# Optimization experiments

Measured on AMD Instinct MI355X. Metric: run time of the kernel, lower is better.

The kernel has to match this reference:

```python
import jax, jax.numpy as jnp
import numpy as np

N, E, B, V, ED, M = 100000, 1600000, 100, 10000, 16, 64
EPS = 1e-5

def _seg_mean(x, ids, n):
    s = jax.ops.segment_sum(x, ids, num_segments=n)
    c = jax.ops.segment_sum(jnp.ones((x.shape[0], 1), x.dtype), ids, num_segments=n)
    return s / jnp.maximum(c, 1.0)

def _graph_conv(x, src, dst, ew, w_rel, b_rel, w_root):
    # PyG GraphConv: out = lin_rel(sum_j e_ji * x_j) + lin_root(x)
    msg = x[src] * ew[:, None]                       # [E, din] gather + weight
    agg = jax.ops.segment_sum(msg, dst, num_segments=x.shape[0])  # scatter-add
    return agg @ w_rel + b_rel + x @ w_root

def _graph_norm(x, batch, g, b, a):
    m = _seg_mean(x, batch, B)
    xc = x - a * m[batch]
    v = _seg_mean(xc * xc, batch, B)
    return g * xc / jnp.sqrt(v[batch] + EPS) + b

def _lrelu(x):
    return jnp.where(x > 0, x, 0.01 * x)

def _bn(x, g, b):
    m = x.mean(0)
    v = x.var(0)
    return g * (x - m) / jnp.sqrt(v + EPS) + b

def setup_inputs() -> dict:
    key = jax.random.key(0)
    ks = jax.random.split(key, 36)
    def lin(k, din, dout):
        return jax.random.normal(k, (din, dout), jnp.float32) / np.sqrt(din)
    d = {
        'x_idx': jax.random.randint(ks[0], (N,), 0, V),
        'edge_index': jax.random.randint(ks[1], (2, E), 0, N),
        'edge_attr': jax.random.uniform(ks[2], (E, 1), jnp.float32),
        'batch': jnp.sort(jax.random.randint(ks[3], (N,), 0, B)),
        'demographics': jax.random.normal(ks[4], (B, 4), jnp.float32),
        'emb': jax.random.normal(ks[5], (V, ED), jnp.float32),
        'w_rel1': lin(ks[6], ED, M),   'b_rel1': jnp.zeros((M,), jnp.float32),   'w_root1': lin(ks[7], ED, M),
        'w_rel2': lin(ks[8], M, 2*M),  'b_rel2': jnp.zeros((2*M,), jnp.float32), 'w_root2': lin(ks[9], M, 2*M),
        'w_rel3': lin(ks[10], 2*M, 4*M),'b_rel3': jnp.zeros((4*M,), jnp.float32),'w_root3': lin(ks[11], 2*M, 4*M),
        'gn1_g': jnp.ones((M,), jnp.float32),   'gn1_b': jnp.zeros((M,), jnp.float32),   'gn1_a': jnp.ones((M,), jnp.float32),
        'gn2_g': jnp.ones((2*M,), jnp.float32), 'gn2_b': jnp.zeros((2*M,), jnp.float32), 'gn2_a': jnp.ones((2*M,), jnp.float32),
        'demo_w': lin(ks[12], 4, 16), 'demo_b': jnp.zeros((16,), jnp.float32),
        'l1_w': lin(ks[13], 4*M + 16, 2*M), 'l1_b': jnp.zeros((2*M,), jnp.float32),
        'bn1_g': jnp.ones((2*M,), jnp.float32), 'bn1_b': jnp.zeros((2*M,), jnp.float32),
        'l2_w': lin(ks[14], 2*M, M), 'l2_b': jnp.zeros((M,), jnp.float32),
        'bn2_g': jnp.ones((M,), jnp.float32), 'bn2_b': jnp.zeros((M,), jnp.float32),
        'l3_w': lin(ks[15], M, 3), 'l3_b': jnp.zeros((3,), jnp.float32),
    }
    return d

def reference(x_idx, edge_index, edge_attr, batch, demographics, emb,
              w_rel1, b_rel1, w_root1, w_rel2, b_rel2, w_root2, w_rel3, b_rel3, w_root3,
              gn1_g, gn1_b, gn1_a, gn2_g, gn2_b, gn2_a,
              demo_w, demo_b, l1_w, l1_b, bn1_g, bn1_b, l2_w, l2_b, bn2_g, bn2_b, l3_w, l3_b):
    src, dst = edge_index[0], edge_index[1]
    ew = edge_attr[:, 0]                  # squeeze(-1)
    x = emb[x_idx]                        # [N, 16]
    x = _graph_conv(x, src, dst, ew, w_rel1, b_rel1, w_root1)
    x = _lrelu(_graph_norm(x, batch, gn1_g, gn1_b, gn1_a))
    x = _graph_conv(x, src, dst, ew, w_rel2, b_rel2, w_root2)
    x = _lrelu(_graph_norm(x, batch, gn2_g, gn2_b, gn2_a))
    x = _graph_conv(x, src, dst, ew, w_rel3, b_rel3, w_root3)   # [N, 256]
    gf = _seg_mean(x, batch, B)                                  # global_mean_pool [B, 256]
    demo = demographics @ demo_w + demo_b                        # [B, 16]
    h = jnp.concatenate([gf, demo], axis=1)                      # [B, 272]
    h = _lrelu(_bn(h @ l1_w + l1_b, bn1_g, bn1_b))               # dropout = identity (eval)
    h = _lrelu(_bn(h @ l2_w + l2_b, bn2_g, bn2_b))
    return h @ l3_w + l3_b                                       # [B, 3]
```

## Files before the change

### kernel.cpp

```cpp
#include <hip/hip_runtime.h>

#define NN 100000
#define NE 1600000
#define NBATCH 100
#define NBUCK 391
constexpr float EPS = 1e-5f;

typedef unsigned short ushort_t;
typedef unsigned int uint_t;

using short8 = __attribute__((ext_vector_type(8))) short;
using floatx4 = __attribute__((ext_vector_type(4))) float;

__device__ __forceinline__ float lrelu(float x) { return x > 0.f ? x : 0.01f * x; }

__device__ __forceinline__ float b2f(ushort_t u) {
    union { uint_t i; float f; } c; c.i = ((uint_t)u) << 16; return c.f;
}
__device__ __forceinline__ ushort_t f2b(float f) {
    union { float f; uint_t i; } c; c.f = f;
    uint_t u = c.i;
    return (ushort_t)((u + 0x7FFFu + ((u >> 16) & 1u)) >> 16);
}
__device__ __forceinline__ void unpack8(const uint4 u, float* f) {
    f[0] = b2f(u.x & 0xffff); f[1] = b2f(u.x >> 16);
    f[2] = b2f(u.y & 0xffff); f[3] = b2f(u.y >> 16);
    f[4] = b2f(u.z & 0xffff); f[5] = b2f(u.z >> 16);
    f[6] = b2f(u.w & 0xffff); f[7] = b2f(u.w >> 16);
}


__global__ __launch_bounds__(256) void k_bcount(const int* __restrict__ dst,
                                                int* __restrict__ bcnt) {
    __shared__ int h[NBUCK];
    for (int i = threadIdx.x; i < NBUCK; i += 256) h[i] = 0;
    __syncthreads();
    for (int e = blockIdx.x * 256 + threadIdx.x; e < NE; e += gridDim.x * 256)
        atomicAdd(&h[dst[e] >> 8], 1);
    __syncthreads();
    for (int i = threadIdx.x; i < NBUCK; i += 256)
        if (h[i]) atomicAdd(&bcnt[i], h[i]);
}

__global__ __launch_bounds__(512) void k_bscan(const int* __restrict__ bcnt,
                                               int* __restrict__ bbase,
                                               int* __restrict__ bcur,
                                               int* __restrict__ rowstart) {
    __shared__ int s[512];
    const int t = threadIdx.x;
    const int v = (t < NBUCK) ? bcnt[t] : 0;
    s[t] = v;
    __syncthreads();
    for (int off = 1; off < 512; off <<= 1) {
        int o = (t >= off) ? s[t - off] : 0;
        __syncthreads();
        s[t] += o;
        __syncthreads();
    }
    const int excl = s[t] - v;
    if (t < NBUCK) { bbase[t] = excl; bcur[t] = excl; }
    if (t == 0) { bbase[NBUCK] = NE; rowstart[NN] = NE; }
}

__global__ __launch_bounds__(256) void k_bscatter(const int* __restrict__ dst,
                                                  const int* __restrict__ srcv,
                                                  const float* __restrict__ ew,
                                                  int* __restrict__ bcur,
                                                  int2* __restrict__ ebuf) {
    __shared__ int h[NBUCK];
    __shared__ int lcur[NBUCK];
    const int chunk = (NE + gridDim.x - 1) / gridDim.x;
    const int beg = blockIdx.x * chunk;
    const int end = (beg + chunk < NE) ? beg + chunk : NE;
    for (int i = threadIdx.x; i < NBUCK; i += 256) h[i] = 0;
    __syncthreads();
    for (int e = beg + threadIdx.x; e < end; e += 256)
        atomicAdd(&h[dst[e] >> 8], 1);
    __syncthreads();
    for (int i = threadIdx.x; i < NBUCK; i += 256)
        lcur[i] = h[i] ? atomicAdd(&bcur[i], h[i]) : 0;
    __syncthreads();
    for (int e = beg + threadIdx.x; e < end; e += 256) {
        const int d = dst[e];
        const int pos = atomicAdd(&lcur[d >> 8], 1);
        ebuf[pos] = make_int2(srcv[e] | ((d & 255) << 20), __float_as_int(ew[e]));
    }
}

__global__ __launch_bounds__(256) void k_bfinal(const int2* __restrict__ ebuf,
                                                const int* __restrict__ bbase,
                                                int* __restrict__ rowstart,
                                                int2* __restrict__ csr_pair) {
    __shared__ int h[256];
    __shared__ int cur[256];
    const int b = blockIdx.x;
    const int t = threadIdx.x;
    const int base = bbase[b];
    const int cnt = bbase[b + 1] - base;
    h[t] = 0;
    __syncthreads();
    for (int i = t; i < cnt; i += 256)
        atomicAdd(&h[(ebuf[base + i].x >> 20) & 255], 1);
    __syncthreads();
    const int v = h[t];
    cur[t] = v;
    __syncthreads();
    for (int off = 1; off < 256; off <<= 1) {
        int o = (t >= off) ? cur[t - off] : 0;
        __syncthreads();
        cur[t] += o;
        __syncthreads();
    }
    const int excl = cur[t] - v;
    const int n = (b << 8) + t;
    if (n < NN) rowstart[n] = base + excl;
    __syncthreads();
    cur[t] = excl;
    __syncthreads();
    for (int i = t; i < cnt; i += 256) {
        const int2 p = ebuf[base + i];
        const int loc = (p.x >> 20) & 255;
        const int pos = base + atomicAdd(&cur[loc], 1);
        csr_pair[pos] = make_int2(p.x & 0xFFFFF, p.y);
    }
}

__global__ void k_bounds(const int* __restrict__ batch, int* __restrict__ bstart) {
    int b = blockIdx.x * blockDim.x + threadIdx.x;
    if (b > NBATCH) return;
    int lo = 0, hi = NN;
    while (lo < hi) {
        int mid = (lo + hi) >> 1;
        if (batch[mid] < b) lo = mid + 1; else hi = mid;
    }
    bstart[b] = lo;
}


__global__ void k_wpack(const float* __restrict__ wr1, const float* __restrict__ wo1,
                        const float* __restrict__ wr2, const float* __restrict__ wo2,
                        const float* __restrict__ wr3, const float* __restrict__ wo3,
                        ushort_t* __restrict__ w1T, ushort_t* __restrict__ w2T,
                        ushort_t* __restrict__ w3T) {
    int idx = blockIdx.x * blockDim.x + threadIdx.x;
    if (idx < 2048) {
        int n = idx >> 5, k = idx & 31;
        float v = (k < 16) ? wr1[k * 64 + n] : wo1[(k - 16) * 64 + n];
        w1T[idx] = f2b(v);
    } else if (idx < 2048 + 16384) {
        int l = idx - 2048; int n = l >> 7, k = l & 127;
        float v = (k < 64) ? wr2[k * 128 + n] : wo2[(k - 64) * 128 + n];
        w2T[l] = f2b(v);
    } else if (idx < 2048 + 16384 + 65536) {
        int l = idx - 18432; int n = l >> 8, k = l & 255;
        float v = (k < 128) ? wr3[k * 256 + n] : wo3[(k - 128) * 256 + n];
        w3T[l] = f2b(v);
    }
}


__global__ void k_gather_b(const int* __restrict__ xi, const float* __restrict__ emb,
                           ushort_t* __restrict__ xcat0) {
    int n = blockIdx.x * blockDim.x + threadIdx.x;
    if (n >= NN) return;
    const float* e = emb + ((size_t)xi[n] << 4);
    uint_t u[8];
#pragma unroll
    for (int j = 0; j < 8; ++j)
        u[j] = (uint_t)f2b(e[2 * j]) | ((uint_t)f2b(e[2 * j + 1]) << 16);
    uint4* o = (uint4*)(xcat0 + (size_t)n * 32 + 16);
    o[0] = {u[0], u[1], u[2], u[3]};
    o[1] = {u[4], u[5], u[6], u[7]};
}


template <int D>
__global__ void k_aggregate_b(ushort_t* __restrict__ xcat, const int2* __restrict__ csr_pair,
                              const int* __restrict__ rowstart) {
    constexpr int LPN = D / 8;
    constexpr int EP = 64 / LPN;
    const int n = blockIdx.x * 4 + (threadIdx.x >> 6);
    const int lane = threadIdx.x & 63;
    const int sl = lane % LPN;
    const int eg = lane / LPN;
    if (n >= NN) return;
    const int beg = rowstart[n], end = rowstart[n + 1];
    float a0[8] = {}, a1[8] = {};
    int i = beg + eg;
    for (; i + EP < end; i += 2 * EP) {
        const int2 p0 = csr_pair[i];
        const int2 p1 = csr_pair[i + EP];
        const float w0 = __int_as_float(p0.y);
        const float w1 = __int_as_float(p1.y);
        const uint4 u0 = *(const uint4*)(xcat + (size_t)p0.x * (2 * D) + D + sl * 8);
        const uint4 u1 = *(const uint4*)(xcat + (size_t)p1.x * (2 * D) + D + sl * 8);
        float f0[8], f1[8];
        unpack8(u0, f0); unpack8(u1, f1);
#pragma unroll
        for (int j = 0; j < 8; ++j) { a0[j] += f0[j] * w0; a1[j] += f1[j] * w1; }
    }
    if (i < end) {
        const int2 p0 = csr_pair[i];
        const float w0 = __int_as_float(p0.y);
        const uint4 u0 = *(const uint4*)(xcat + (size_t)p0.x * (2 * D) + D + sl * 8);
        float f0[8];
        unpack8(u0, f0);
#pragma unroll
        for (int j = 0; j < 8; ++j) a0[j] += f0[j] * w0;
    }
#pragma unroll
    for (int j = 0; j < 8; ++j) a0[j] += a1[j];
#pragma unroll
    for (int m = LPN; m < 64; m <<= 1)
#pragma unroll
        for (int j = 0; j < 8; ++j) a0[j] += __shfl_xor(a0[j], m);
    if (eg == 0) {
        uint_t u[4];
#pragma unroll
        for (int j = 0; j < 4; ++j)
            u[j] = (uint_t)f2b(a0[2 * j]) | ((uint_t)f2b(a0[2 * j + 1]) << 16);
        *(uint4*)(xcat + (size_t)n * (2 * D) + sl * 8) = {u[0], u[1], u[2], u[3]};
    }
}


template <int K2, int DOUT, bool BOUT>
__global__ __launch_bounds__(256) void k_conv_mfma(
        const ushort_t* __restrict__ xcat, const ushort_t* __restrict__ wcatT,
        const float* __restrict__ brel, void* __restrict__ outp) {
    constexpr int CW = DOUT / 64;
    const int lane = threadIdx.x & 63;
    const int wv = threadIdx.x >> 6;
    const int m = lane & 15;
    const int quad = lane >> 4;
    const int r0 = blockIdx.x * 64;

    floatx4 acc[4][CW] = {};

    const ushort_t* arow[4];
#pragma unroll
    for (int r = 0; r < 4; ++r) {
        int an = r0 + r * 16 + m; if (an >= NN) an = NN - 1;
        arow[r] = xcat + (size_t)an * K2 + quad * 8;
    }
    const ushort_t* brow[CW];
#pragma unroll
    for (int c = 0; c < CW; ++c)
        brow[c] = wcatT + (size_t)((wv * CW + c) * 16 + m) * K2 + quad * 8;

    for (int kk = 0; kk < K2; kk += 32) {
        short8 a[4], b[CW];
#pragma unroll
        for (int r = 0; r < 4; ++r) a[r] = *(const short8*)(arow[r] + kk);
#pragma unroll
        for (int c = 0; c < CW; ++c) b[c] = *(const short8*)(brow[c] + kk);
#pragma unroll
        for (int r = 0; r < 4; ++r)
#pragma unroll
            for (int c = 0; c < CW; ++c)
                acc[r][c] = __builtin_amdgcn_mfma_f32_16x16x32_bf16(a[r], b[c], acc[r][c], 0, 0, 0);
    }

#pragma unroll
    for (int c = 0; c < CW; ++c) {
        const int col = (wv * CW + c) * 16 + m;
        const float bias = brel[col];
#pragma unroll
        for (int r = 0; r < 4; ++r) {
#pragma unroll
            for (int rr = 0; rr < 4; ++rr) {
                const int row = r0 + r * 16 + quad * 4 + rr;
                if (row < NN) {
                    const float v = acc[r][c][rr] + bias;
                    if constexpr (BOUT) ((ushort_t*)outp)[(size_t)row * DOUT + col] = f2b(v);
                    else                ((float*)outp)[(size_t)row * DOUT + col] = v;
                }
            }
        }
    }
}


template <int D, int OST>
__global__ __launch_bounds__(256) void k_graphnorm(
        const float* __restrict__ xf, ushort_t* __restrict__ xout,
        const int* __restrict__ bstart, const float* __restrict__ a,
        const float* __restrict__ g, const float* __restrict__ bb) {
    __shared__ float4 reds[256];
    __shared__ float4 redq[256];
    __shared__ float smean[64];
    __shared__ float sinv[64];
    const int b = blockIdx.x;
    const int col0 = blockIdx.y * 64;
    const int c4 = (threadIdx.x & 15) * 4;
    const int rg = threadIdx.x >> 4;
    const int beg = bstart[b], end = bstart[b + 1];
    const float cntf = fmaxf((float)(end - beg), 1.f);

    float4 s = {0.f, 0.f, 0.f, 0.f}, q = {0.f, 0.f, 0.f, 0.f};
    for (int r = beg + rg; r < end; r += 16) {
        const float4 v = *(const float4*)&xf[(size_t)r * D + col0 + c4];
        s.x += v.x; s.y += v.y; s.z += v.z; s.w += v.w;
        q.x += v.x * v.x; q.y += v.y * v.y; q.z += v.z * v.z; q.w += v.w * v.w;
    }
    reds[threadIdx.x] = s;
    redq[threadIdx.x] = q;
    __syncthreads();
    if (rg == 0) {
        float4 S = reds[threadIdx.x], Q = redq[threadIdx.x];
        for (int k = 1; k < 16; ++k) {
            const float4 s2 = reds[threadIdx.x + 16 * k];
            const float4 q2 = redq[threadIdx.x + 16 * k];
            S.x += s2.x; S.y += s2.y; S.z += s2.z; S.w += s2.w;
            Q.x += q2.x; Q.y += q2.y; Q.z += q2.z; Q.w += q2.w;
        }
        const float4 al = *(const float4*)&a[col0 + c4];
        const float Sv[4] = {S.x, S.y, S.z, S.w};
        const float Qv[4] = {Q.x, Q.y, Q.z, Q.w};
        const float av[4] = {al.x, al.y, al.z, al.w};
#pragma unroll
        for (int c = 0; c < 4; ++c) {
            const float mm = Sv[c] / cntf;
            const float ex2 = Qv[c] / cntf;
            const float var = fmaxf(ex2 - mm * mm * (2.f * av[c] - av[c] * av[c]), 0.f);
            smean[c4 + c] = mm;
            sinv[c4 + c] = 1.f / sqrtf(var + EPS);
        }
    }
    __syncthreads();
    const float4 mean4 = *(const float4*)&smean[c4];
    const float4 inv4 = *(const float4*)&sinv[c4];
    const float4 al4 = *(const float4*)&a[col0 + c4];
    const float4 g4 = *(const float4*)&g[col0 + c4];
    const float4 bb4 = *(const float4*)&bb[col0 + c4];
    for (int r = beg + rg; r < end; r += 16) {
        const float4 v = *(const float4*)&xf[(size_t)r * D + col0 + c4];
        float y0 = lrelu(g4.x * (v.x - al4.x * mean4.x) * inv4.x + bb4.x);
        float y1 = lrelu(g4.y * (v.y - al4.y * mean4.y) * inv4.y + bb4.y);
        float y2 = lrelu(g4.z * (v.z - al4.z * mean4.z) * inv4.z + bb4.z);
        float y3 = lrelu(g4.w * (v.w - al4.w * mean4.w) * inv4.w + bb4.w);
        uint2 o;
        o.x = (uint_t)f2b(y0) | ((uint_t)f2b(y1) << 16);
        o.y = (uint_t)f2b(y2) | ((uint_t)f2b(y3) << 16);
        *(uint2*)&xout[(size_t)r * OST + col0 + c4] = o;
    }
}


__global__ __launch_bounds__(256) void k_gf2b(const ushort_t* __restrict__ x3b,
                                              const int* __restrict__ bstart,
                                              float* __restrict__ h0) {
    __shared__ float4 red[256];
    const int b = blockIdx.x;
    const int col0 = blockIdx.y * 64;
    const int c4 = (threadIdx.x & 15) * 4;
    const int rg = threadIdx.x >> 4;
    const int beg = bstart[b], end = bstart[b + 1];
    const float cntf = fmaxf((float)(end - beg), 1.f);
    float4 s = {0.f, 0.f, 0.f, 0.f};
    for (int r = beg + rg; r < end; r += 16) {
        const uint2 u = *(const uint2*)&x3b[(size_t)r * 256 + col0 + c4];
        s.x += b2f(u.x & 0xffff); s.y += b2f(u.x >> 16);
        s.z += b2f(u.y & 0xffff); s.w += b2f(u.y >> 16);
    }
    red[threadIdx.x] = s;
    __syncthreads();
    if (rg == 0) {
        float4 S = red[threadIdx.x];
        for (int k = 1; k < 16; ++k) {
            const float4 s2 = red[threadIdx.x + 16 * k];
            S.x += s2.x; S.y += s2.y; S.z += s2.z; S.w += s2.w;
        }
        S.x /= cntf; S.y /= cntf; S.z /= cntf; S.w /= cntf;
        *(float4*)&h0[b * 272 + col0 + c4] = S;
    }
}

__global__ void k_demo(const float* __restrict__ dg, const float* __restrict__ w,
                       const float* __restrict__ b, float* __restrict__ h0) {
    int idx = blockIdx.x * blockDim.x + threadIdx.x;
    if (idx < NBATCH * 16) {
        int i = idx >> 4, j = idx & 15;
        float acc = b[j];
        for (int k = 0; k < 4; ++k) acc += dg[i * 4 + k] * w[k * 16 + j];
        h0[i * 272 + 256 + j] = acc;
    }
}

__global__ __launch_bounds__(128) void k_lin_bn(const float* __restrict__ in,
                                                const float* __restrict__ w,
                                                const float* __restrict__ bias,
                                                const float* __restrict__ g,
                                                const float* __restrict__ bb,
                                                float* __restrict__ out,
                                                int rows, int K, int C) {
    __shared__ float s1[128], s2[128];
    const int j = blockIdx.x;
    const int t = threadIdx.x;
    float v = 0.f;
    if (t < rows) {
        v = bias[j];
        for (int k = 0; k < K; ++k) v += in[t * K + k] * w[k * C + j];
    }
    s1[t] = (t < rows) ? v : 0.f;
    s2[t] = (t < rows) ? v * v : 0.f;
    __syncthreads();
    for (int off = 64; off > 0; off >>= 1) {
        if (t < off) { s1[t] += s1[t + off]; s2[t] += s2[t + off]; }
        __syncthreads();
    }
    const float m = s1[0] / rows;
    const float var = fmaxf(s2[0] / rows - m * m, 0.f);
    const float inv = 1.f / sqrtf(var + EPS);
    if (t < rows) out[t * C + j] = lrelu(g[j] * (v - m) * inv + bb[j]);
}

__global__ void k_linear(const float* __restrict__ in, const float* __restrict__ w,
                         const float* __restrict__ b, float* __restrict__ out,
                         int rows, int K, int D) {
    int total = rows * D;
    for (int idx = blockIdx.x * blockDim.x + threadIdx.x; idx < total; idx += gridDim.x * blockDim.x) {
        int i = idx / D, j = idx - i * D;
        float acc = b[j];
        for (int k = 0; k < K; ++k) acc += in[i * K + k] * w[k * D + j];
        out[idx] = acc;
    }
}


extern "C" void kernel_launch(void* const* d_in, const int* in_sizes, int n_in,
                              void* d_out, int out_size, void* d_ws, size_t ws_size,
                              hipStream_t stream) {
    const int*   x_idx  = (const int*)d_in[0];
    const int*   ei     = (const int*)d_in[1];
    const float* eattr  = (const float*)d_in[2];
    const int*   batch  = (const int*)d_in[3];
    const float* demog  = (const float*)d_in[4];
    const float* emb    = (const float*)d_in[5];
    const float* wrel1  = (const float*)d_in[6];
    const float* brel1  = (const float*)d_in[7];
    const float* wroot1 = (const float*)d_in[8];
    const float* wrel2  = (const float*)d_in[9];
    const float* brel2  = (const float*)d_in[10];
    const float* wroot2 = (const float*)d_in[11];
    const float* wrel3  = (const float*)d_in[12];
    const float* brel3  = (const float*)d_in[13];
    const float* wroot3 = (const float*)d_in[14];
    const float* gn1g = (const float*)d_in[15];
    const float* gn1b = (const float*)d_in[16];
    const float* gn1a = (const float*)d_in[17];
    const float* gn2g = (const float*)d_in[18];
    const float* gn2b = (const float*)d_in[19];
    const float* gn2a = (const float*)d_in[20];
    const float* dw   = (const float*)d_in[21];
    const float* db   = (const float*)d_in[22];
    const float* l1w  = (const float*)d_in[23];
    const float* l1b  = (const float*)d_in[24];
    const float* bn1g = (const float*)d_in[25];
    const float* bn1b = (const float*)d_in[26];
    const float* l2w  = (const float*)d_in[27];
    const float* l2b  = (const float*)d_in[28];
    const float* bn2g = (const float*)d_in[29];
    const float* bn2b = (const float*)d_in[30];
    const float* l3w  = (const float*)d_in[31];
    const float* l3b  = (const float*)d_in[32];
    float* out = (float*)d_out;

    float*    W     = (float*)d_ws;
    float*    xf    = W;
    int2*     ebuf  = (int2*)W;
    ushort_t* x3b   = (ushort_t*)(W + 12800000);
    ushort_t* xcat0 = (ushort_t*)(W + 25600000);
    ushort_t* xcat1 = (ushort_t*)(W + 27200000);
    ushort_t* xcat2 = (ushort_t*)(W + 33600000);
    ushort_t* w1T   = (ushort_t*)(W + 46400000);
    ushort_t* w2T   = w1T + 2048;
    ushort_t* w3T   = w2T + 16384;
    int2*     csr_pair = (int2*)(W + 46450000);
    int*      rowstart = (int*)(W + 49650000);
    int*      bstart   = (int*)(W + 49760000);
    int*      bcnt     = (int*)(W + 49761000);
    int*      bbase    = (int*)(W + 49762000);
    int*      bcur     = (int*)(W + 49763000);
    float*    h0 = W + 49770000;
    float*    h1 = h0 + 27200;
    float*    h2 = h1 + 12800;

    const int* src = ei;
    const int* dst = ei + NE;

    auto gsz = [](long long t) {
        long long b = (t + 255) / 256;
        return (int)(b > 524288 ? 524288 : b);
    };
    const int mfma_blk = (NN + 63) / 64;
    const int nagg_blk = (NN + 3) / 4;

    hipMemsetAsync(bcnt, 0, NBUCK * sizeof(int), stream);
    k_bcount<<<256, 256, 0, stream>>>(dst, bcnt);
    k_bscan<<<1, 512, 0, stream>>>(bcnt, bbase, bcur, rowstart);
    k_bscatter<<<256, 256, 0, stream>>>(dst, src, eattr, bcur, ebuf);
    k_bfinal<<<NBUCK, 256, 0, stream>>>(ebuf, bbase, rowstart, csr_pair);

    k_bounds<<<1, 128, 0, stream>>>(batch, bstart);
    k_wpack<<<(83968 + 255) / 256, 256, 0, stream>>>(wrel1, wroot1, wrel2, wroot2, wrel3, wroot3,
                                                     w1T, w2T, w3T);

    k_gather_b<<<(NN + 255) / 256, 256, 0, stream>>>(x_idx, emb, xcat0);

    k_aggregate_b<16><<<nagg_blk, 256, 0, stream>>>(xcat0, csr_pair, rowstart);
    k_conv_mfma<32, 64, false><<<mfma_blk, 256, 0, stream>>>(xcat0, w1T, brel1, xf);
    k_graphnorm<64, 128><<<dim3(NBATCH, 1), 256, 0, stream>>>(xf, xcat1 + 64, bstart, gn1a, gn1g, gn1b);

    k_aggregate_b<64><<<nagg_blk, 256, 0, stream>>>(xcat1, csr_pair, rowstart);
    k_conv_mfma<128, 128, false><<<mfma_blk, 256, 0, stream>>>(xcat1, w2T, brel2, xf);
    k_graphnorm<128, 256><<<dim3(NBATCH, 2), 256, 0, stream>>>(xf, xcat2 + 128, bstart, gn2a, gn2g, gn2b);

    k_aggregate_b<128><<<nagg_blk, 256, 0, stream>>>(xcat2, csr_pair, rowstart);
    k_conv_mfma<256, 256, true><<<mfma_blk, 256, 0, stream>>>(xcat2, w3T, brel3, x3b);

    k_gf2b<<<dim3(NBATCH, 4), 256, 0, stream>>>(x3b, bstart, h0);
    k_demo<<<(NBATCH * 16 + 255) / 256, 256, 0, stream>>>(demog, dw, db, h0);
    k_lin_bn<<<128, 128, 0, stream>>>(h0, l1w, l1b, bn1g, bn1b, h1, NBATCH, 272, 128);
    k_lin_bn<<<64, 128, 0, stream>>>(h1, l2w, l2b, bn2g, bn2b, h2, NBATCH, 128, 64);
    k_linear<<<gsz(NBATCH * 3), 256, 0, stream>>>(h2, l3w, l3b, out, NBATCH, 64, 3);
}
```

Before: 714.3 us.

## Fuse global mean pool into final conv MFMA epilogue via atomics

```diff
diff --git a/kernel.cpp b/kernel.cpp
--- a/kernel.cpp
+++ b/kernel.cpp
@@ -224,10 +224,12 @@
 }
 
 
-template <int K2, int DOUT, bool BOUT>
+template <int K2, int DOUT, int MODE>
 __global__ __launch_bounds__(256) void k_conv_mfma(
         const ushort_t* __restrict__ xcat, const ushort_t* __restrict__ wcatT,
-        const float* __restrict__ brel, void* __restrict__ outp) {
+        const float* __restrict__ brel, float* __restrict__ outp,
+        const int* __restrict__ batch, const int* __restrict__ bstart,
+        float* __restrict__ gfacc) {
     constexpr int CW = DOUT / 64;
     const int lane = threadIdx.x & 63;
     const int wv = threadIdx.x >> 6;
@@ -261,23 +263,65 @@
                 acc[r][c] = __builtin_amdgcn_mfma_f32_16x16x32_bf16(a[r], b[c], acc[r][c], 0, 0, 0);
     }
 
-#pragma unroll
-    for (int c = 0; c < CW; ++c) {
-        const int col = (wv * CW + c) * 16 + m;
-        const float bias = brel[col];
-#pragma unroll
-        for (int r = 0; r < 4; ++r) {
-#pragma unroll
-            for (int rr = 0; rr < 4; ++rr) {
-                const int row = r0 + r * 16 + quad * 4 + rr;
-                if (row < NN) {
-                    const float v = acc[r][c][rr] + bias;
-                    if constexpr (BOUT) ((ushort_t*)outp)[(size_t)row * DOUT + col] = f2b(v);
-                    else                ((float*)outp)[(size_t)row * DOUT + col] = v;
+    float bias[CW];
+#pragma unroll
+    for (int c = 0; c < CW; ++c) bias[c] = brel[(wv * CW + c) * 16 + m];
+
+    if constexpr (MODE == 0) {
+#pragma unroll
+        for (int c = 0; c < CW; ++c) {
+            const int col = (wv * CW + c) * 16 + m;
+#pragma unroll
+            for (int r = 0; r < 4; ++r)
+#pragma unroll
+                for (int rr = 0; rr < 4; ++rr) {
+                    const int row = r0 + r * 16 + quad * 4 + rr;
+                    if (row < NN)
+                        outp[(size_t)row * DOUT + col] = acc[r][c][rr] + bias[c];
                 }
+        }
+    } else {
+        const int rtop = (r0 + 63 < NN) ? r0 + 63 : NN - 1;
+        const int sb0 = batch[r0];
+        const int sb1 = batch[rtop];
+        for (int sb = sb0; sb <= sb1; ++sb) {
+            const int lo = (bstart[sb] > r0) ? bstart[sb] : r0;
+            int hi = bstart[sb + 1];
+            if (hi > r0 + 64) hi = r0 + 64;
+            float s[CW];
+#pragma unroll
+            for (int c = 0; c < CW; ++c) s[c] = 0.f;
+#pragma unroll
+            for (int r = 0; r < 4; ++r)
+#pragma unroll
+                for (int rr = 0; rr < 4; ++rr) {
+                    const int row = r0 + r * 16 + quad * 4 + rr;
+                    if (row >= lo && row < hi) {
+#pragma unroll
+                        for (int c = 0; c < CW; ++c) s[c] += acc[r][c][rr] + bias[c];
+                    }
+                }
+#pragma unroll
+            for (int c = 0; c < CW; ++c) {
+                s[c] += __shfl_xor(s[c], 16);
+                s[c] += __shfl_xor(s[c], 32);
+            }
+            if (quad == 0) {
+#pragma unroll
+                for (int c = 0; c < CW; ++c)
+                    atomicAdd(&gfacc[sb * 256 + (wv * CW + c) * 16 + m], s[c]);
             }
         }
     }
+}
+
+__global__ void k_gffin(const float* __restrict__ gfacc, const int* __restrict__ bstart,
+                        float* __restrict__ h0) {
+    int idx = blockIdx.x * blockDim.x + threadIdx.x;
+    if (idx >= NBATCH * 256) return;
+    int b = idx >> 8, c = idx & 255;
+    float cnt = fmaxf((float)(bstart[b + 1] - bstart[b]), 1.f);
+    h0[b * 272 + c] = gfacc[idx] / cnt;
 }
 
 
@@ -343,36 +387,6 @@
         o.x = (uint_t)f2b(y0) | ((uint_t)f2b(y1) << 16);
         o.y = (uint_t)f2b(y2) | ((uint_t)f2b(y3) << 16);
         *(uint2*)&xout[(size_t)r * OST + col0 + c4] = o;
-    }
-}
-
-
-__global__ __launch_bounds__(256) void k_gf2b(const ushort_t* __restrict__ x3b,
-                                              const int* __restrict__ bstart,
-                                              float* __restrict__ h0) {
-    __shared__ float4 red[256];
-    const int b = blockIdx.x;
-    const int col0 = blockIdx.y * 64;
-    const int c4 = (threadIdx.x & 15) * 4;
-    const int rg = threadIdx.x >> 4;
-    const int beg = bstart[b], end = bstart[b + 1];
-    const float cntf = fmaxf((float)(end - beg), 1.f);
-    float4 s = {0.f, 0.f, 0.f, 0.f};
-    for (int r = beg + rg; r < end; r += 16) {
-        const uint2 u = *(const uint2*)&x3b[(size_t)r * 256 + col0 + c4];
-        s.x += b2f(u.x & 0xffff); s.y += b2f(u.x >> 16);
-        s.z += b2f(u.y & 0xffff); s.w += b2f(u.y >> 16);
-    }
-    red[threadIdx.x] = s;
-    __syncthreads();
-    if (rg == 0) {
-        float4 S = red[threadIdx.x];
-        for (int k = 1; k < 16; ++k) {
-            const float4 s2 = red[threadIdx.x + 16 * k];
-            S.x += s2.x; S.y += s2.y; S.z += s2.z; S.w += s2.w;
-        }
-        S.x /= cntf; S.y /= cntf; S.z /= cntf; S.w /= cntf;
-        *(float4*)&h0[b * 272 + col0 + c4] = S;
     }
 }
 
@@ -469,7 +483,7 @@
     float*    W     = (float*)d_ws;
     float*    xf    = W;
     int2*     ebuf  = (int2*)W;
-    ushort_t* x3b   = (ushort_t*)(W + 12800000);
+    float*    gfacc = W + 12800000;
     ushort_t* xcat0 = (ushort_t*)(W + 25600000);
     ushort_t* xcat1 = (ushort_t*)(W + 27200000);
     ushort_t* xcat2 = (ushort_t*)(W + 33600000);
@@ -505,21 +519,22 @@
     k_bounds<<<1, 128, 0, stream>>>(batch, bstart);
     k_wpack<<<(83968 + 255) / 256, 256, 0, stream>>>(wrel1, wroot1, wrel2, wroot2, wrel3, wroot3,
                                                      w1T, w2T, w3T);
+    hipMemsetAsync(gfacc, 0, NBATCH * 256 * sizeof(float), stream);
 
     k_gather_b<<<(NN + 255) / 256, 256, 0, stream>>>(x_idx, emb, xcat0);
 
     k_aggregate_b<16><<<nagg_blk, 256, 0, stream>>>(xcat0, csr_pair, rowstart);
-    k_conv_mfma<32, 64, false><<<mfma_blk, 256, 0, stream>>>(xcat0, w1T, brel1, xf);
+    k_conv_mfma<32, 64, 0><<<mfma_blk, 256, 0, stream>>>(xcat0, w1T, brel1, xf, batch, bstart, nullptr);
     k_graphnorm<64, 128><<<dim3(NBATCH, 1), 256, 0, stream>>>(xf, xcat1 + 64, bstart, gn1a, gn1g, gn1b);
 
     k_aggregate_b<64><<<nagg_blk, 256, 0, stream>>>(xcat1, csr_pair, rowstart);
-    k_conv_mfma<128, 128, false><<<mfma_blk, 256, 0, stream>>>(xcat1, w2T, brel2, xf);
+    k_conv_mfma<128, 128, 0><<<mfma_blk, 256, 0, stream>>>(xcat1, w2T, brel2, xf, batch, bstart, nullptr);
     k_graphnorm<128, 256><<<dim3(NBATCH, 2), 256, 0, stream>>>(xf, xcat2 + 128, bstart, gn2a, gn2g, gn2b);
 
     k_aggregate_b<128><<<nagg_blk, 256, 0, stream>>>(xcat2, csr_pair, rowstart);
-    k_conv_mfma<256, 256, true><<<mfma_blk, 256, 0, stream>>>(xcat2, w3T, brel3, x3b);
-
-    k_gf2b<<<dim3(NBATCH, 4), 256, 0, stream>>>(x3b, bstart, h0);
+    k_conv_mfma<256, 256, 2><<<mfma_blk, 256, 0, stream>>>(xcat2, w3T, brel3, nullptr, batch, bstart, gfacc);
+
+    k_gffin<<<(NBATCH * 256 + 255) / 256, 256, 0, stream>>>(gfacc, bstart, h0);
     k_demo<<<(NBATCH * 16 + 255) / 256, 256, 0, stream>>>(demog, dw, db, h0);
     k_lin_bn<<<128, 128, 0, stream>>>(h0, l1w, l1b, bn1g, bn1b, h1, NBATCH, 272, 128);
     k_lin_bn<<<64, 128, 0, stream>>>(h1, l2w, l2b, bn2g, bn2b, h2, NBATCH, 128, 64);
```

New measurement: 668.3 us. 6.4% less time.
